# Kernel tuning notes

Measured on AMD Instinct MI355X. Metric: run time of the kernel, lower is better.

## Reference

```python
import jax, jax.numpy as jnp
import numpy as np

B, T, N, D = 8, 512, 64, 128
PRED, HEADS, HID = 96, 8, 256
KERNELS = (17, 49)
NUM_LAYERS = 1
NUM_BLOCKS = 1
IDX_T = np.arange(64)   # lowest 64 of T//2=256 rfft modes (mode_select='low')
IDX_C = np.arange(32)   # min(modes, (N+1)//2)=32 lowest channel-frequency modes


def _mov_avg(x, k):
    # x: [B, T, N]; replicate-pad (k-1)//2 on both ends, then box filter (AvgPool1d stride 1)
    pad = (k - 1) // 2
    xp = jnp.concatenate([jnp.repeat(x[:, :1], pad, axis=1), x, jnp.repeat(x[:, -1:], pad, axis=1)], axis=1)
    c = jnp.cumsum(xp, axis=1)
    c = jnp.concatenate([jnp.zeros_like(c[:, :1]), c], axis=1)
    return (c[:, k:] - c[:, :-k]) / k


def _decomp_multi(x, dec_w, dec_b):
    # series_decomp_multi: softmax-weighted mixture of moving averages
    mm = jnp.stack([_mov_avg(x, k) for k in KERNELS], axis=-1)        # [B,T,N,K]
    w = jax.nn.softmax(x[..., None] * dec_w + dec_b, axis=-1)         # Linear(1,K) on x, softmax over K
    trend = jnp.sum(mm * w, axis=-1)
    return x - trend, trend


def _complex_attn(x, Wq, Wk, Wv, Wo):
    # x: complex64 [B, L, M, D]; multi-head attention over the M selected frequency modes.
    # Real projection weights applied to complex activations; attention weights are
    # softmax over |q k^H| / sqrt(dh); values stay complex.
    Bq, L, M, Dm = x.shape
    dh = Dm // HEADS
    q = jnp.einsum('blmd,de->blme', x, Wq).reshape(Bq, L, M, HEADS, dh)
    k = jnp.einsum('blmd,de->blme', x, Wk).reshape(Bq, L, M, HEADS, dh)
    v = jnp.einsum('blmd,de->blme', x, Wv).reshape(Bq, L, M, HEADS, dh)
    s = jnp.einsum('blmhd,blnhd->blhmn', q, jnp.conj(k))              # complex scores
    w = jax.nn.softmax(jnp.abs(s) / np.sqrt(dh), axis=-1)             # real attn weights
    o = jnp.einsum('blhmn,blnhd->blmhd', w.astype(x.dtype), v).reshape(Bq, L, M, Dm)
    return jnp.einsum('blmd,de->blme', o, Wo)


def _cem(x, Wq, Wk, Wv, Wo):
    # channel-frequency attention; x: [B, N, T, D]
    xp = jnp.transpose(x, (0, 2, 1, 3))                               # [B,T,N,D]
    xf = jnp.fft.rfft(xp, axis=2)                                     # [B,T,N//2+1,D]
    xs = xf[:, :, IDX_C, :]                                           # gather selected modes
    for _ in range(NUM_LAYERS):
        xs = _complex_attn(xs, Wq, Wk, Wv, Wo)
    yf = jnp.zeros((x.shape[0], T, N // 2 + 1, D), dtype=xf.dtype).at[:, :, IDX_C, :].set(xs)
    y = jnp.fft.irfft(yf, n=N, axis=2)
    return jnp.transpose(y, (0, 2, 1, 3))


def _tem(x, Wq, Wk, Wv, Wo):
    # temporal-frequency attention; x: [B, N, T, D]
    xf = jnp.fft.rfft(x, axis=2)                                      # [B,N,T//2+1,D]
    xs = xf[:, :, IDX_T, :]
    for _ in range(NUM_LAYERS):
        xs = _complex_attn(xs, Wq, Wk, Wv, Wo)
    yf = jnp.zeros((x.shape[0], N, T // 2 + 1, D), dtype=xf.dtype).at[:, :, IDX_T, :].set(xs)
    return jnp.fft.irfft(yf, n=T, axis=2)


def setup_inputs() -> dict:
    key = jax.random.key(0)
    ks = jax.random.split(key, 24)
    r = lambda i, shape, s: jax.random.normal(ks[i], shape, jnp.float32) * s
    K = len(KERNELS)
    return {
        'x': jax.random.normal(ks[0], (B, T, N), jnp.float32),
        'embeddings': jax.random.normal(ks[1], (1, D), jnp.float32),
        'dec_w': r(2, (K,), 1.0),
        'dec_b': jnp.zeros((K,), jnp.float32),
        'mlp_w1': r(3, (T, HID), 1.0 / np.sqrt(T)),
        'mlp_b1': jnp.zeros((HID,), jnp.float32),
        'mlp_w2': r(4, (HID, HID), 1.0 / np.sqrt(HID)),
        'mlp_b2': jnp.zeros((HID,), jnp.float32),
        'mlp_w3': r(5, (HID, PRED), 1.0 / np.sqrt(HID)),
        'mlp_b3': jnp.zeros((PRED,), jnp.float32),
        'cem_Wq': r(6, (D, D), 0.02), 'cem_Wk': r(7, (D, D), 0.02),
        'cem_Wv': r(8, (D, D), 0.02), 'cem_Wo': r(9, (D, D), 0.02),
        'tem_Wq': r(10, (D, D), 0.02), 'tem_Wk': r(11, (D, D), 0.02),
        'tem_Wv': r(12, (D, D), 0.02), 'tem_Wo': r(13, (D, D), 0.02),
        'dr_w': r(14, (D, 1), 1.0 / np.sqrt(D)),
        'dr_b': jnp.zeros((1,), jnp.float32),
        'out_w': r(15, (T, PRED), 1.0 / np.sqrt(T)),
        'out_b': jnp.zeros((PRED,), jnp.float32),
        'W_fuse': jnp.ones((2,), jnp.float32),
    }


def reference(x, embeddings, dec_w, dec_b, mlp_w1, mlp_b1, mlp_w2, mlp_b2, mlp_w3, mlp_b3,
              cem_Wq, cem_Wk, cem_Wv, cem_Wo, tem_Wq, tem_Wk, tem_Wv, tem_Wo,
              dr_w, dr_b, out_w, out_b, W_fuse):
    res, trend = _decomp_multi(x, dec_w, dec_b)
    t = jnp.transpose(trend, (0, 2, 1))                               # [B,N,T]
    h = jax.nn.relu(t @ mlp_w1 + mlp_b1)
    h = jax.nn.relu(h @ mlp_w2 + mlp_b2)
    trend_out = jnp.transpose(h @ mlp_w3 + mlp_b3, (0, 2, 1))         # [B,PRED,N]
    # tokenEmb: [B,T,N] -> [B,N,T,1] * [1,D]
    xe = jnp.transpose(res, (0, 2, 1))[..., None] * embeddings[0]      # [B,N,T,D]
    for _ in range(NUM_BLOCKS):
        xe = _cem(xe, cem_Wq, cem_Wk, cem_Wv, cem_Wo)
    for _ in range(NUM_BLOCKS):
        xe = _tem(xe, tem_Wq, tem_Wk, tem_Wv, tem_Wo)
    xr = jnp.einsum('bntd,do->bnto', xe, dr_w)[..., 0] + dr_b[0]      # dim_reduction -> [B,N,T]
    xo = jnp.transpose(jnp.einsum('bnt,tp->bnp', xr, out_w) + out_b, (0, 2, 1))  # [B,PRED,N]
    return W_fuse[0] * xo + W_fuse[1] * trend_out
```

## Files before the change

### kernel.cpp

```cpp
#include <hip/hip_runtime.h>
#include <hip/hip_bf16.h>

typedef __hip_bfloat16 bf16;
typedef float v2f __attribute__((ext_vector_type(2)));

constexpr int CB = 8;
constexpr int CT = 512;
constexpr int CN = 64;
constexpr int CD = 128;
constexpr int CP = 96;
constexpr int CH = 8;
constexpr int CDH = 16;
constexpr int CHID = 256;
constexpr int CM = 32;
constexpr int CG = 64;
constexpr float TWO_PI = 6.28318530717958647692f;

__device__ __forceinline__ float LD(const void* p, size_t i, bool f) {
  return f ? ((const float*)p)[i] : __bfloat162float(((const bf16*)p)[i]);
}
template <bool F32>
__device__ __forceinline__ float LDT(const void* p, size_t i) {
  return F32 ? ((const float*)p)[i] : __bfloat162float(((const bf16*)p)[i]);
}

__device__ __forceinline__ bool detect_f32(const void* x) {
  const unsigned int* xw = (const unsigned int*)x;
  unsigned int w = xw[threadIdx.x & 63];
  unsigned int e = (w >> 7) & 0xFF;
  unsigned long long m = __ballot(e >= 0x90 || e <= 0x60);
  return __popcll(m) > 3;
}

struct MArgs {
  const void *x, *dec_w, *dec_b, *out_w, *emb, *cWq, *cWk, *cWv, *cWo;
  const void *tWq, *tWk, *tWv, *tWo, *drw, *drb, *out_b, *wfuse;
  const void *w1, *b1, *w2, *b2, *w3, *b3;
  float *trendo, *Pbuf, *ewq, *ewk, *ewv, *wod, *owr, *owi;
  void* out;
};

template <bool F32>
__device__ void k2_body(float* sm, const MArgs& a) {
  float* xbuf = sm;
  float* rows = sm + 2560;
  float* h1 = sm + 4608;
  float* h2 = sm + 5632;
  int r0 = blockIdx.x * 4;
  int b = r0 >> 6, n0 = r0 & 63;
  int tid = threadIdx.x;
  size_t xb = (size_t)b * CT * CN + n0;
  for (int i = tid; i < CT * 4; i += 256) {
    int t = i >> 2, q = i & 3;
    xbuf[t * 5 + q] = LDT<F32>(a.x, xb + (size_t)t * CN + q);
  }
  __syncthreads();
  {
    float w0 = LDT<F32>(a.dec_w, 0), w1 = LDT<F32>(a.dec_w, 1);
    float c0 = LDT<F32>(a.dec_b, 0), c1 = LDT<F32>(a.dec_b, 1);
    int q = tid & 3, tl = tid >> 2;
    int t0 = tl * 8;
    float s17 = 0.f, s49 = 0.f;
    #pragma unroll
    for (int o = -8; o <= 8; ++o) {
      int u = t0 + o; u = u < 0 ? 0 : (u > CT - 1 ? CT - 1 : u);
      s17 += xbuf[u * 5 + q];
    }
    #pragma unroll
    for (int o = -24; o <= 24; ++o) {
      int u = t0 + o; u = u < 0 ? 0 : (u > CT - 1 ? CT - 1 : u);
      s49 += xbuf[u * 5 + q];
    }
    #pragma unroll
    for (int k = 0; k < 8; ++k) {
      int t = t0 + k;
      if (k > 0) {
        int up8 = t + 8 > CT - 1 ? CT - 1 : t + 8;
        int dn9 = t - 9 < 0 ? 0 : t - 9;
        int up24 = t + 24 > CT - 1 ? CT - 1 : t + 24;
        int dn25 = t - 25 < 0 ? 0 : t - 25;
        s17 += xbuf[up8 * 5 + q] - xbuf[dn9 * 5 + q];
        s49 += xbuf[up24 * 5 + q] - xbuf[dn25 * 5 + q];
      }
      float m0 = s17 * (1.f / 17.f), m1 = s49 * (1.f / 49.f);
      float xv = xbuf[t * 5 + q];
      float l0 = xv * w0 + c0, l1 = xv * w1 + c1;
      float mx = fmaxf(l0, l1);
      float e0 = __expf(l0 - mx), e1 = __expf(l1 - mx);
      rows[q * CT + t] = (e0 * m0 + e1 * m1) / (e0 + e1);
    }
  }
  __syncthreads();
  int c = tid;
  float a0, a1, a2, a3;
  {
    float bias = LDT<F32>(a.b1, c);
    a0 = a1 = a2 = a3 = 0.f;
    #pragma unroll 16
    for (int t = 0; t < CT; ++t) {
      float w = LDT<F32>(a.w1, t * CHID + c);
      a0 += rows[0 * CT + t] * w; a1 += rows[1 * CT + t] * w;
      a2 += rows[2 * CT + t] * w; a3 += rows[3 * CT + t] * w;
    }
    h1[0 * CHID + c] = fmaxf(a0 + bias, 0.f); h1[1 * CHID + c] = fmaxf(a1 + bias, 0.f);
    h1[2 * CHID + c] = fmaxf(a2 + bias, 0.f); h1[3 * CHID + c] = fmaxf(a3 + bias, 0.f);
  }
  __syncthreads();
  {
    float bias = LDT<F32>(a.b2, c);
    a0 = a1 = a2 = a3 = 0.f;
    #pragma unroll 16
    for (int i = 0; i < CHID; ++i) {
      float w = LDT<F32>(a.w2, i * CHID + c);
      a0 += h1[0 * CHID + i] * w; a1 += h1[1 * CHID + i] * w;
      a2 += h1[2 * CHID + i] * w; a3 += h1[3 * CHID + i] * w;
    }
    h2[0 * CHID + c] = fmaxf(a0 + bias, 0.f); h2[1 * CHID + c] = fmaxf(a1 + bias, 0.f);
    h2[2 * CHID + c] = fmaxf(a2 + bias, 0.f); h2[3 * CHID + c] = fmaxf(a3 + bias, 0.f);
  }
  __syncthreads();
  if (tid < 2 * CP) {
    int p = tid < CP ? tid : tid - CP;
    int qh = tid < CP ? 0 : 2;
    float bias = LDT<F32>(a.b3, p);
    a0 = a1 = 0.f;
    #pragma unroll 16
    for (int i = 0; i < CHID; ++i) {
      float w = LDT<F32>(a.w3, i * CP + p);
      a0 += h2[qh * CHID + i] * w; a1 += h2[(qh + 1) * CHID + i] * w;
    }
    a.trendo[((size_t)(b * CN + n0 + qh)) * CP + p] = a0 + bias;
    a.trendo[((size_t)(b * CN + n0 + qh + 1)) * CP + p] = a1 + bias;
  }
}

__global__ __launch_bounds__(256, 4) void kS2(MArgs a) {
  __shared__ __align__(16) float sm[6656];
  bool f32 = detect_f32(a.x);
  int blk = blockIdx.x, tid = threadIdx.x;
  if (blk < 128) {
    if (f32) k2_body<true>(sm, a);
    else     k2_body<false>(sm, a);
  } else if (blk < 1152) {
    float* xl = sm;
    float* rowl = sm + 3328;
    float* Rr = sm + 3584;
    float* Ri = sm + 3712;
    float* aR = sm + 3840;
    float2* SL = (float2*)(sm + 3968);
    float* prod = sm + 6016;
    float* chl = sm + 6144;
    float* eml = sm + 6152;
    int bk = blk - 128;
    int b = bk >> 7, tbase = (bk & 127) * 4;
    int w = tid >> 6, lane = tid & 63;
    size_t xb = (size_t)b * CT * CN;
    for (int i = tid; i < 52 * 64; i += 256) {
      int r = i >> 6, n = i & 63;
      int u = tbase - 24 + r; u = u < 0 ? 0 : (u > CT - 1 ? CT - 1 : u);
      xl[i] = LD(a.x, xb + (size_t)u * CN + n, f32);
    }
    if (tid < 128) eml[tid] = LD(a.emb, tid, f32);
    __syncthreads();
    {
      float* chp = (float*)SL;
      const void* Wm = (w < 2) ? a.cWq : a.cWk;
      int d0 = (w & 1) * 64;
      float p0 = 0.f, p1 = 0.f;
      #pragma unroll 16
      for (int d = d0; d < d0 + 64; ++d) {
        float em = eml[d];
        p0 = fmaf(em, LD(Wm, (size_t)d * CD + lane, f32), p0);
        p1 = fmaf(em, LD(Wm, (size_t)d * CD + 64 + lane, f32), p1);
      }
      chp[w * 128 + lane] = p0;
      chp[w * 128 + 64 + lane] = p1;
    }
    __syncthreads();
    if (tid < 128) {
      float* chp = (float*)SL;
      float pq = chp[tid] + chp[128 + tid];
      float pk = chp[256 + tid] + chp[384 + tid];
      prod[tid] = pq * pk;
    }
    __syncthreads();
    if (tid < CH) {
      float s = 0;
      #pragma unroll
      for (int j = 0; j < 16; ++j) s += prod[tid * 16 + j];
      chl[tid] = fabsf(s);
    }
    {
      int Lt = 24 + w;
      float w0 = LD(a.dec_w, 0, f32), w1 = LD(a.dec_w, 1, f32);
      float c0 = LD(a.dec_b, 0, f32), c1 = LD(a.dec_b, 1, f32);
      float s17 = 0;
      #pragma unroll
      for (int o = -8; o <= 8; ++o) s17 += xl[(Lt + o) * 64 + lane];
      float s49 = 0;
      #pragma unroll
      for (int o = -24; o <= 24; ++o) s49 += xl[(Lt + o) * 64 + lane];
      float m0 = s17 * (1.f / 17.f), m1 = s49 * (1.f / 49.f);
      float xv = xl[Lt * 64 + lane];
      float l0 = xv * w0 + c0, l1 = xv * w1 + c1;
      float mx = fmaxf(l0, l1);
      float e0 = __expf(l0 - mx), e1 = __expf(l1 - mx);
      float tr = (e0 * m0 + e1 * m1) / (e0 + e1);
      rowl[w * 64 + lane] = xv - tr;
    }
    __syncthreads();
    if (lane < CM) {
      float cf, sf;
      sincosf((float)lane * (TWO_PI / CN), &sf, &cf);
      float wr = 1.f, wi = 0.f, rr = 0.f, ri = 0.f;
      #pragma unroll 8
      for (int n2 = 0; n2 < CN; ++n2) {
        float xv = rowl[w * 64 + n2];
        rr = fmaf(xv, wr, rr); ri = fmaf(-xv, wi, ri);
        float nr = wr * cf - wi * sf; wi = wi * cf + wr * sf; wr = nr;
      }
      Rr[w * 32 + lane] = rr; Ri[w * 32 + lane] = ri;
      aR[w * 32 + lane] = sqrtf(rr * rr + ri * ri);
    }
    __syncthreads();
    float amax = 0;
    for (int m = 0; m < CM; ++m) amax = fmaxf(amax, aR[w * 32 + m]);
    #pragma unroll
    for (int i = 0; i < 4; ++i) {
      int pair = lane + 64 * i;
      int h = pair >> 5, m = pair & 31;
      float alpha = 0.25f * chl[h] * aR[w * 32 + m];
      float den = 0, sr = 0, si = 0;
      for (int n2 = 0; n2 < CM; ++n2) {
        float e = __expf(alpha * (aR[w * 32 + n2] - amax));
        den += e; sr += e * Rr[w * 32 + n2]; si += e * Ri[w * 32 + n2];
      }
      SL[w * 256 + pair] = make_float2(sr / den, si / den);
    }
    __syncthreads();
    {
      int n2 = lane, t = tbase + w;
      const float2* Sw = SL + w * 256;
      float acc[8];
      #pragma unroll
      for (int h = 0; h < CH; ++h) acc[h] = Sw[h * 32].x;
      float cd, sd;
      sincosf((float)n2 * (TWO_PI / CN), &sd, &cd);
      float px = cd, py = sd;
      for (int f = 1; f < CM; ++f) {
        #pragma unroll
        for (int h = 0; h < CH; ++h) {
          float2 s = Sw[h * 32 + f];
          acc[h] += 2.f * (s.x * px - s.y * py);
        }
        float nx = px * cd - py * sd; py = py * cd + px * sd; px = nx;
      }
      float* Pb = a.Pbuf + (((size_t)(b * CN + n2)) * CT + t) * CH;
      ((float4*)Pb)[0] = make_float4(acc[0] * (1.f / CN), acc[1] * (1.f / CN),
                                     acc[2] * (1.f / CN), acc[3] * (1.f / CN));
      ((float4*)Pb)[1] = make_float4(acc[4] * (1.f / CN), acc[5] * (1.f / CN),
                                     acc[6] * (1.f / CN), acc[7] * (1.f / CN));
    }
  } else if (blk < 1216) {
    float* ps = sm;
    int g = blk - 1152;
    int tc = tid >> 7, idx = tid & 127;
    if (idx < CP) {
      int p = idx, t0 = tc * 256;
      float s0, c0v, ss, cs;
      sincosf((float)((g * t0) & (CT - 1)) * (TWO_PI / CT), &s0, &c0v);
      sincosf((float)g * (TWO_PI / CT), &ss, &cs);
      float wr = c0v, wi = s0, ar = 0.f, ai = 0.f;
      #pragma unroll 16
      for (int t = 0; t < 256; ++t) {
        float w = LD(a.out_w, (size_t)(t0 + t) * CP + p, f32);
        ar = fmaf(w, wr, ar); ai = fmaf(w, wi, ai);
        float nr = wr * cs - wi * ss; wi = wi * cs + wr * ss; wr = nr;
      }
      ps[(tc * CP + p) * 2] = ar; ps[(tc * CP + p) * 2 + 1] = ai;
    }
    __syncthreads();
    if (tid < CP) {
      a.owr[g * CP + tid] = ps[tid * 2] + ps[(CP + tid) * 2];
      a.owi[g * CP + tid] = ps[tid * 2 + 1] + ps[(CP + tid) * 2 + 1];
    }
  } else if (blk < 1228) {
    float* eml = sm;
    float* evl = sm + 128;
    float* ewoh = sm + 160;
    int bi = blk - 1216;
    int half = tid >> 7, e = tid & 127;
    int pairIdx = bi * 2 + half;
    int which = pairIdx >> 3, h = pairIdx & 7;
    if (tid < 128) eml[tid] = LD(a.emb, tid, f32);
    __syncthreads();
    if (e < 16) {
      float acc = 0;
      #pragma unroll 8
      for (int d = 0; d < CD; ++d) acc += eml[d] * LD(a.cWv, d * CD + h * CDH + e, f32);
      evl[half * 16 + e] = acc;
    }
    __syncthreads();
    {
      float acc = 0;
      #pragma unroll
      for (int j = 0; j < CDH; ++j)
        acc += evl[half * 16 + j] * LD(a.cWo, (h * CDH + j) * CD + e, f32);
      ewoh[half * 128 + e] = acc;
    }
    __syncthreads();
    {
      const void* W = which == 0 ? a.tWq : (which == 1 ? a.tWk : a.tWv);
      float acc = 0;
      #pragma unroll 8
      for (int d = 0; d < CD; ++d) acc += ewoh[half * 128 + d] * LD(W, d * CD + e, f32);
      (which == 0 ? a.ewq : (which == 1 ? a.ewk : a.ewv))[h * CD + e] = acc;
    }
  } else {
    float* drl = sm;
    if (tid < 128) drl[tid] = LD(a.drw, tid, f32);
    __syncthreads();
    if (tid < 128) {
      float acc = 0;
      #pragma unroll 8
      for (int d = 0; d < CD; ++d) acc += LD(a.tWo, tid * CD + d, f32) * drl[d];
      a.wod[tid] = acc;
    }
  }
}

__global__ __launch_bounds__(512, 4) void kC(MArgs a) {
  __shared__ __align__(16) float sm[8128];
  float* Pl = sm;
  float* QL = sm + 4352;
  float* Cl = sm + 5376;
  float* Ul = sm + 5888;
  float2* vdL = (float2*)(sm + 5952);
  float2* zL = (float2*)(sm + 6976);
  float* zrow = sm + 8000;
  bool f32 = detect_f32(a.x);
  int blk = blockIdx.x, tid = threadIdx.x;
  int b = blk >> 6, n = blk & 63;
  const float4* src4 = (const float4*)(a.Pbuf + ((size_t)(b * CN + n)) * CT * CH);
  for (int i = tid; i < 1024; i += 512) {
    float4 v = src4[i];
    int t = i >> 1, half = i & 1;
    int k = t >> 6, u = t & 63;
    float* dst = Pl + u * 68 + half * 32 + k;
    dst[0] = v.x; dst[8] = v.y; dst[16] = v.z; dst[24] = v.w;
  }
  for (int id = tid; id < 512 + 64; id += 512) {
    if (id < 512) {
      int h = id >> 6, aa = (id >> 3) & 7, b2 = id & 7;
      float c = 0;
      #pragma unroll
      for (int j = 0; j < CDH; ++j)
        c += a.ewq[aa * CD + h * CDH + j] * a.ewk[b2 * CD + h * CDH + j];
      Cl[id] = c;
    } else {
      int r = id - 512;
      int h = r >> 3, aa = r & 7;
      float c = 0;
      #pragma unroll
      for (int j = 0; j < CDH; ++j) c += a.ewv[aa * CD + h * CDH + j] * a.wod[h * CDH + j];
      Ul[r] = c;
    }
  }
  __syncthreads();
  {
    int g = tid >> 3, h = tid & 7;
    float cs, sn;
    sincosf((float)g * (TWO_PI / CT), &sn, &cs);
    float wr = 1.f, wi = 0.f;
    float car[8] = {0, 0, 0, 0, 0, 0, 0, 0};
    float cai[8] = {0, 0, 0, 0, 0, 0, 0, 0};
    #pragma unroll 4
    for (int u = 0; u < 64; ++u) {
      const float4* pu = (const float4*)(Pl + u * 68 + h * 8);
      float4 lo = pu[0], hi = pu[1];
      car[0] = fmaf(lo.x, wr, car[0]); cai[0] = fmaf(lo.x, wi, cai[0]);
      car[1] = fmaf(lo.y, wr, car[1]); cai[1] = fmaf(lo.y, wi, cai[1]);
      car[2] = fmaf(lo.z, wr, car[2]); cai[2] = fmaf(lo.z, wi, cai[2]);
      car[3] = fmaf(lo.w, wr, car[3]); cai[3] = fmaf(lo.w, wi, cai[3]);
      car[4] = fmaf(hi.x, wr, car[4]); cai[4] = fmaf(hi.x, wi, cai[4]);
      car[5] = fmaf(hi.y, wr, car[5]); cai[5] = fmaf(hi.y, wi, cai[5]);
      car[6] = fmaf(hi.z, wr, car[6]); cai[6] = fmaf(hi.z, wi, cai[6]);
      car[7] = fmaf(hi.w, wr, car[7]); cai[7] = fmaf(hi.w, wi, cai[7]);
      float nr = wr * cs + wi * sn; wi = wi * cs - wr * sn; wr = nr;
    }
    float cs8, sn8;
    sincosf((float)(g & 7) * (TWO_PI / 8.f), &sn8, &cs8);
    float pr = 1.f, pi = 0.f, qr = 0.f, qi = 0.f;
    #pragma unroll
    for (int k = 0; k < 8; ++k) {
      qr += car[k] * pr - cai[k] * pi;
      qi += cai[k] * pr + car[k] * pi;
      float nr2 = pr * cs8 + pi * sn8; pi = pi * cs8 - pr * sn8; pr = nr2;
    }
    QL[g * 16 + h * 2] = qr;
    QL[g * 16 + h * 2 + 1] = qi;
  }
  __syncthreads();
  int h = tid >> 6, m = tid & 63;
  v2f qp[8];
  {
    const v2f* qrow = (const v2f*)(QL + m * 16);
    #pragma unroll
    for (int j = 0; j < 8; ++j) qp[j] = qrow[j];
  }
  {
    float vr = 0, vi = 0;
    #pragma unroll
    for (int aa = 0; aa < 8; ++aa) {
      float u = Ul[h * 8 + aa];
      vr = fmaf(qp[aa].x, u, vr); vi = fmaf(qp[aa].y, u, vi);
    }
    vdL[h * 64 + m] = make_float2(vr, vi);
  }
  v2f uu[8], vv[8];
  #pragma unroll
  for (int bb = 0; bb < 8; ++bb) {
    v2f acc = {0.f, 0.f};
    #pragma unroll
    for (int aa = 0; aa < 8; ++aa) acc += qp[aa] * Cl[(h * 8 + aa) * 8 + bb];
    uu[bb] = acc;
    vv[bb] = (v2f){acc.y, -acc.x};
  }
  __syncthreads();
  float mx = -1e30f, den = 0.f, zr = 0.f, zi = 0.f;
  #pragma unroll 4
  for (int g = 0; g < CG; ++g) {
    const v2f* y = (const v2f*)(QL + g * 16);
    v2f sr2 = {0.f, 0.f}, si2 = {0.f, 0.f};
    #pragma unroll
    for (int j = 0; j < 8; ++j) {
      v2f yj = y[j];
      sr2 = uu[j] * yj + sr2;
      si2 = vv[j] * yj + si2;
    }
    float sr = sr2.x + sr2.y;
    float si = si2.x + si2.y;
    float s = 0.25f * sqrtf(sr * sr + si * si);
    if (s > mx) {
      float f = __expf(mx - s);
      den *= f; zr *= f; zi *= f; mx = s;
    }
    float e = __expf(s - mx);
    float2 vd = vdL[h * 64 + g];
    den += e; zr += e * vd.x; zi += e * vd.y;
  }
  {
    float rv = 1.f / den;
    zL[h * 64 + m] = make_float2(zr * rv, zi * rv);
  }
  __syncthreads();
  if (tid < 128) {
    int g = tid >> 1, c = tid & 1;
    float acc = 0;
    #pragma unroll
    for (int hh = 0; hh < CH; ++hh) acc += c ? zL[hh * 64 + g].y : zL[hh * 64 + g].x;
    zrow[g * 2 + c] = acc;
  }
  __syncthreads();
  if (tid < CP) {
    int p = tid;
    float acc = zrow[0] * a.owr[p] - zrow[1] * a.owi[p];
    #pragma unroll 8
    for (int g = 1; g < CG; ++g)
      acc += 2.f * (zrow[g * 2] * a.owr[g * CP + p] - zrow[g * 2 + 1] * a.owi[g * CP + p]);
    float xo = acc * (1.f / CT) + LD(a.drb, 0, f32) * a.owr[p] + LD(a.out_b, p, f32);
    float val = LD(a.wfuse, 0, f32) * xo
              + LD(a.wfuse, 1, f32) * a.trendo[((size_t)(b * CN + n)) * CP + p];
    size_t oidx = ((size_t)(b * CP + p)) * CN + n;
    if (f32) ((float*)a.out)[oidx] = val;
    else ((bf16*)a.out)[oidx] = __float2bfloat16(val);
  }
}

extern "C" void kernel_launch(void* const* d_in, const int* in_sizes, int n_in,
                              void* d_out, int out_size, void* d_ws, size_t ws_size,
                              hipStream_t stream) {
  float* W = (float*)d_ws;
  MArgs a;
  a.x = d_in[0];   a.emb = d_in[1];  a.dec_w = d_in[2]; a.dec_b = d_in[3];
  a.w1 = d_in[4];  a.b1 = d_in[5];   a.w2 = d_in[6];    a.b2 = d_in[7];
  a.w3 = d_in[8];  a.b3 = d_in[9];
  a.cWq = d_in[10]; a.cWk = d_in[11]; a.cWv = d_in[12]; a.cWo = d_in[13];
  a.tWq = d_in[14]; a.tWk = d_in[15]; a.tWv = d_in[16]; a.tWo = d_in[17];
  a.drw = d_in[18]; a.drb = d_in[19]; a.out_w = d_in[20]; a.out_b = d_in[21];
  a.wfuse = d_in[22];
  a.trendo = W; W += (size_t)CB * CN * CP;
  a.Pbuf = W;   W += (size_t)CB * CN * CT * CH;
  a.ewq = W;    W += CH * CD;
  a.ewk = W;    W += CH * CD;
  a.ewv = W;    W += CH * CD;
  a.wod = W;    W += CD;
  a.owr = W;    W += CG * CP;
  a.owi = W;    W += CG * CP;
  a.out = d_out;

  kS2<<<1229, 256, 0, stream>>>(a);
  kC<<<512, 512, 0, stream>>>(a);
}
```

Baseline: 184.6 us.

## Halve trend-MLP rows per block, shrink LDS, and use all lanes for channel DFT

```diff
diff --git a/kernel.cpp b/kernel.cpp
--- a/kernel.cpp
+++ b/kernel.cpp
@@ -43,115 +43,116 @@
 template <bool F32>
 __device__ void k2_body(float* sm, const MArgs& a) {
   float* xbuf = sm;
-  float* rows = sm + 2560;
-  float* h1 = sm + 4608;
-  float* h2 = sm + 5632;
-  int r0 = blockIdx.x * 4;
+  float* rows = sm;
+  float* h1 = sm + 1536;
+  float* h2 = sm + 2048;
+  int r0 = blockIdx.x * 2;
   int b = r0 >> 6, n0 = r0 & 63;
   int tid = threadIdx.x;
   size_t xb = (size_t)b * CT * CN + n0;
-  for (int i = tid; i < CT * 4; i += 256) {
-    int t = i >> 2, q = i & 3;
-    xbuf[t * 5 + q] = LDT<F32>(a.x, xb + (size_t)t * CN + q);
-  }
-  __syncthreads();
+  for (int i = tid; i < CT * 2; i += 256) {
+    int t = i >> 1, q = i & 1;
+    xbuf[t * 3 + q] = LDT<F32>(a.x, xb + (size_t)t * CN + q);
+  }
+  __syncthreads();
+  float trv[4];
+  int q = tid & 1, tl = tid >> 1, t0 = tl * 4;
   {
     float w0 = LDT<F32>(a.dec_w, 0), w1 = LDT<F32>(a.dec_w, 1);
     float c0 = LDT<F32>(a.dec_b, 0), c1 = LDT<F32>(a.dec_b, 1);
-    int q = tid & 3, tl = tid >> 2;
-    int t0 = tl * 8;
     float s17 = 0.f, s49 = 0.f;
     #pragma unroll
     for (int o = -8; o <= 8; ++o) {
       int u = t0 + o; u = u < 0 ? 0 : (u > CT - 1 ? CT - 1 : u);
-      s17 += xbuf[u * 5 + q];
+      s17 += xbuf[u * 3 + q];
     }
     #pragma unroll
     for (int o = -24; o <= 24; ++o) {
       int u = t0 + o; u = u < 0 ? 0 : (u > CT - 1 ? CT - 1 : u);
-      s49 += xbuf[u * 5 + q];
-    }
-    #pragma unroll
-    for (int k = 0; k < 8; ++k) {
+      s49 += xbuf[u * 3 + q];
+    }
+    #pragma unroll
+    for (int k = 0; k < 4; ++k) {
       int t = t0 + k;
       if (k > 0) {
         int up8 = t + 8 > CT - 1 ? CT - 1 : t + 8;
         int dn9 = t - 9 < 0 ? 0 : t - 9;
         int up24 = t + 24 > CT - 1 ? CT - 1 : t + 24;
         int dn25 = t - 25 < 0 ? 0 : t - 25;
-        s17 += xbuf[up8 * 5 + q] - xbuf[dn9 * 5 + q];
-        s49 += xbuf[up24 * 5 + q] - xbuf[dn25 * 5 + q];
+        s17 += xbuf[up8 * 3 + q] - xbuf[dn9 * 3 + q];
+        s49 += xbuf[up24 * 3 + q] - xbuf[dn25 * 3 + q];
       }
       float m0 = s17 * (1.f / 17.f), m1 = s49 * (1.f / 49.f);
-      float xv = xbuf[t * 5 + q];
+      float xv = xbuf[t * 3 + q];
       float l0 = xv * w0 + c0, l1 = xv * w1 + c1;
       float mx = fmaxf(l0, l1);
       float e0 = __expf(l0 - mx), e1 = __expf(l1 - mx);
-      rows[q * CT + t] = (e0 * m0 + e1 * m1) / (e0 + e1);
-    }
-  }
+      trv[k] = (e0 * m0 + e1 * m1) / (e0 + e1);
+    }
+  }
+  __syncthreads();
+  #pragma unroll
+  for (int k = 0; k < 4; ++k) rows[q * CT + t0 + k] = trv[k];
   __syncthreads();
   int c = tid;
-  float a0, a1, a2, a3;
+  float a0, a1;
   {
     float bias = LDT<F32>(a.b1, c);
-    a0 = a1 = a2 = a3 = 0.f;
+    a0 = a1 = 0.f;
     #pragma unroll 16
     for (int t = 0; t < CT; ++t) {
       float w = LDT<F32>(a.w1, t * CHID + c);
-      a0 += rows[0 * CT + t] * w; a1 += rows[1 * CT + t] * w;
-      a2 += rows[2 * CT + t] * w; a3 += rows[3 * CT + t] * w;
-    }
-    h1[0 * CHID + c] = fmaxf(a0 + bias, 0.f); h1[1 * CHID + c] = fmaxf(a1 + bias, 0.f);
-    h1[2 * CHID + c] = fmaxf(a2 + bias, 0.f); h1[3 * CHID + c] = fmaxf(a3 + bias, 0.f);
+      a0 = fmaf(rows[t], w, a0);
+      a1 = fmaf(rows[CT + t], w, a1);
+    }
+    h1[c] = fmaxf(a0 + bias, 0.f);
+    h1[CHID + c] = fmaxf(a1 + bias, 0.f);
   }
   __syncthreads();
   {
     float bias = LDT<F32>(a.b2, c);
-    a0 = a1 = a2 = a3 = 0.f;
+    a0 = a1 = 0.f;
     #pragma unroll 16
     for (int i = 0; i < CHID; ++i) {
       float w = LDT<F32>(a.w2, i * CHID + c);
-      a0 += h1[0 * CHID + i] * w; a1 += h1[1 * CHID + i] * w;
-      a2 += h1[2 * CHID + i] * w; a3 += h1[3 * CHID + i] * w;
-    }
-    h2[0 * CHID + c] = fmaxf(a0 + bias, 0.f); h2[1 * CHID + c] = fmaxf(a1 + bias, 0.f);
-    h2[2 * CHID + c] = fmaxf(a2 + bias, 0.f); h2[3 * CHID + c] = fmaxf(a3 + bias, 0.f);
+      a0 = fmaf(h1[i], w, a0);
+      a1 = fmaf(h1[CHID + i], w, a1);
+    }
+    h2[c] = fmaxf(a0 + bias, 0.f);
+    h2[CHID + c] = fmaxf(a1 + bias, 0.f);
   }
   __syncthreads();
   if (tid < 2 * CP) {
     int p = tid < CP ? tid : tid - CP;
-    int qh = tid < CP ? 0 : 2;
+    int qh = tid < CP ? 0 : 1;
     float bias = LDT<F32>(a.b3, p);
-    a0 = a1 = 0.f;
+    a0 = 0.f;
     #pragma unroll 16
-    for (int i = 0; i < CHID; ++i) {
-      float w = LDT<F32>(a.w3, i * CP + p);
-      a0 += h2[qh * CHID + i] * w; a1 += h2[(qh + 1) * CHID + i] * w;
-    }
+    for (int i = 0; i < CHID; ++i)
+      a0 = fmaf(h2[qh * CHID + i], LDT<F32>(a.w3, i * CP + p), a0);
     a.trendo[((size_t)(b * CN + n0 + qh)) * CP + p] = a0 + bias;
-    a.trendo[((size_t)(b * CN + n0 + qh + 1)) * CP + p] = a1 + bias;
   }
 }
 
 __global__ __launch_bounds__(256, 4) void kS2(MArgs a) {
-  __shared__ __align__(16) float sm[6656];
+  __shared__ __align__(16) float sm[4608];
   bool f32 = detect_f32(a.x);
   int blk = blockIdx.x, tid = threadIdx.x;
-  if (blk < 128) {
+  if (blk < 256) {
     if (f32) k2_body<true>(sm, a);
     else     k2_body<false>(sm, a);
-  } else if (blk < 1152) {
+  } else if (blk < 1280) {
     float* xl = sm;
+    float2* SL = (float2*)sm;
+    float* chp = sm + 3328;
     float* rowl = sm + 3328;
     float* Rr = sm + 3584;
     float* Ri = sm + 3712;
     float* aR = sm + 3840;
-    float2* SL = (float2*)(sm + 3968);
-    float* prod = sm + 6016;
-    float* chl = sm + 6144;
-    float* eml = sm + 6152;
-    int bk = blk - 128;
+    float* prod = sm + 3968;
+    float* chl = sm + 4096;
+    float* eml = sm + 4104;
+    int bk = blk - 256;
     int b = bk >> 7, tbase = (bk & 127) * 4;
     int w = tid >> 6, lane = tid & 63;
     size_t xb = (size_t)b * CT * CN;
@@ -163,7 +164,6 @@
     if (tid < 128) eml[tid] = LD(a.emb, tid, f32);
     __syncthreads();
     {
-      float* chp = (float*)SL;
       const void* Wm = (w < 2) ? a.cWq : a.cWk;
       int d0 = (w & 1) * 64;
       float p0 = 0.f, p1 = 0.f;
@@ -178,7 +178,6 @@
     }
     __syncthreads();
     if (tid < 128) {
-      float* chp = (float*)SL;
       float pq = chp[tid] + chp[128 + tid];
       float pk = chp[256 + tid] + chp[384 + tid];
       prod[tid] = pq * pk;
@@ -209,33 +208,46 @@
       rowl[w * 64 + lane] = xv - tr;
     }
     __syncthreads();
-    if (lane < CM) {
+    float am, amax;
+    {
+      int m = lane & 31, half = lane >> 5;
       float cf, sf;
-      sincosf((float)lane * (TWO_PI / CN), &sf, &cf);
-      float wr = 1.f, wi = 0.f, rr = 0.f, ri = 0.f;
+      sincosf((float)m * (TWO_PI / CN), &sf, &cf);
+      float wr = (half & m & 1) ? -1.f : 1.f, wi = 0.f;
+      float rr = 0.f, ri = 0.f;
+      const float* rw = rowl + w * 64 + half * 32;
       #pragma unroll 8
-      for (int n2 = 0; n2 < CN; ++n2) {
-        float xv = rowl[w * 64 + n2];
-        rr = fmaf(xv, wr, rr); ri = fmaf(-xv, wi, ri);
+      for (int j = 0; j < 32; ++j) {
+        float xv = rw[j];
+        rr = fmaf(xv, wr, rr);
+        ri = fmaf(-xv, wi, ri);
         float nr = wr * cf - wi * sf; wi = wi * cf + wr * sf; wr = nr;
       }
-      Rr[w * 32 + lane] = rr; Ri[w * 32 + lane] = ri;
-      aR[w * 32 + lane] = sqrtf(rr * rr + ri * ri);
-    }
-    __syncthreads();
-    float amax = 0;
-    for (int m = 0; m < CM; ++m) amax = fmaxf(amax, aR[w * 32 + m]);
-    #pragma unroll
-    for (int i = 0; i < 4; ++i) {
-      int pair = lane + 64 * i;
-      int h = pair >> 5, m = pair & 31;
-      float alpha = 0.25f * chl[h] * aR[w * 32 + m];
-      float den = 0, sr = 0, si = 0;
-      for (int n2 = 0; n2 < CM; ++n2) {
-        float e = __expf(alpha * (aR[w * 32 + n2] - amax));
-        den += e; sr += e * Rr[w * 32 + n2]; si += e * Ri[w * 32 + n2];
+      rr += __shfl_xor(rr, 32);
+      ri += __shfl_xor(ri, 32);
+      am = sqrtf(rr * rr + ri * ri);
+      if (half == 0) { Rr[w * 32 + m] = rr; Ri[w * 32 + m] = ri; aR[w * 32 + m] = am; }
+      amax = am;
+      #pragma unroll
+      for (int s2 = 1; s2 < 32; s2 <<= 1) amax = fmaxf(amax, __shfl_xor(amax, s2));
+    }
+    __syncthreads();
+    {
+      float base = 0.25f * am;
+      #pragma unroll
+      for (int i = 0; i < 4; ++i) {
+        int pair = lane + 64 * i;
+        int h = pair >> 5;
+        float alpha = chl[h] * base;
+        float den = 0, sr = 0, si = 0;
+        for (int n2 = 0; n2 < CM; ++n2) {
+          float e = __expf(alpha * (aR[w * 32 + n2] - amax));
+          den += e;
+          sr = fmaf(e, Rr[w * 32 + n2], sr);
+          si = fmaf(e, Ri[w * 32 + n2], si);
+        }
+        SL[w * 256 + pair] = make_float2(sr / den, si / den);
       }
-      SL[w * 256 + pair] = make_float2(sr / den, si / den);
     }
     __syncthreads();
     {
@@ -261,9 +273,9 @@
       ((float4*)Pb)[1] = make_float4(acc[4] * (1.f / CN), acc[5] * (1.f / CN),
                                      acc[6] * (1.f / CN), acc[7] * (1.f / CN));
     }
-  } else if (blk < 1216) {
+  } else if (blk < 1344) {
     float* ps = sm;
-    int g = blk - 1152;
+    int g = blk - 1280;
     int tc = tid >> 7, idx = tid & 127;
     if (idx < CP) {
       int p = idx, t0 = tc * 256;
@@ -284,11 +296,11 @@
       a.owr[g * CP + tid] = ps[tid * 2] + ps[(CP + tid) * 2];
       a.owi[g * CP + tid] = ps[tid * 2 + 1] + ps[(CP + tid) * 2 + 1];
     }
-  } else if (blk < 1228) {
+  } else if (blk < 1356) {
     float* eml = sm;
     float* evl = sm + 128;
     float* ewoh = sm + 160;
-    int bi = blk - 1216;
+    int bi = blk - 1344;
     int half = tid >> 7, e = tid & 127;
     int pairIdx = bi * 2 + half;
     int which = pairIdx >> 3, h = pairIdx & 7;
@@ -499,6 +511,6 @@
   a.owi = W;    W += CG * CP;
   a.out = d_out;
 
-  kS2<<<1229, 256, 0, stream>>>(a);
+  kS2<<<1357, 256, 0, stream>>>(a);
   kC<<<512, 512, 0, stream>>>(a);
 }
```

After: 185.8 us. Within noise of the previous version (+0.7%).
